# Kernel optimization log

Hardware: AMD Instinct MI355X
Metric: run time of the kernel (lower is better)

Reference implementation:

```python
import jax, jax.numpy as jnp
import numpy as np
import math

B, L = 2, 512
D_MODEL = 64
N_HEAD = 8
N_GLOBAL = 64
N_ITER = 2
DISTS = 4
K_RANK = 4
REG_H = 1.0
REG_Z = 1.0
NEG = -1e9


def setup_inputs() -> dict:
    key = jax.random.key(0)
    k1, k2, k3, k4 = jax.random.split(key, 4)
    x = jax.random.normal(k1, (B, L, D_MODEL), dtype=jnp.float32)
    mask = jnp.ones((B, L), dtype=jnp.int32)
    # nn.init.normal_ defaults (std=1)
    distribution_params = jax.random.normal(k2, (2 * DISTS, K_RANK), dtype=jnp.float32)
    ternary = jax.random.normal(k3, (K_RANK, D_MODEL, D_MODEL, N_HEAD), dtype=jnp.float32)
    # global_: std = 1/sqrt(d_model), single-channel -> heads dim = 1
    global_param = jax.random.normal(k4, (N_GLOBAL, D_MODEL, 1), dtype=jnp.float32) * (1.0 / math.sqrt(D_MODEL))
    return {"x": x, "mask": mask, "distribution_params": distribution_params,
            "ternary": ternary, "global_param": global_param}


def _softmax(s):
    return jax.nn.softmax(s, axis=-1)


def _distmask(distribution_params, n, dtype):
    # distance(i,j) = clip(i - j, -dists, dists); row 0 of params is zeros (distance 0)
    dist = jnp.arange(n)[:, None] - jnp.arange(n)[None, :]
    dist = jnp.clip(dist, -DISTS, DISTS)
    params = jnp.concatenate([jnp.zeros((1, K_RANK), dtype), distribution_params], axis=0)  # [2*dists+1, k]
    # torch negative indexing wraps; emulate explicitly
    idx = jnp.where(dist < 0, dist + 2 * DISTS + 1, dist)
    return params[idx].transpose(2, 0, 1)  # [k, n, n]


def reference(x, mask, distribution_params, ternary, global_param):
    bsz, n, d = x.shape
    mask1d = mask != 0                                   # [B, L]
    mask2d = mask1d[:, :, None] & mask1d[:, None, :]     # [B, L, L]
    inv2d = ~mask2d[:, None, :, :]                       # [B, 1, L, L] broadcast over heads
    inv1d = ~mask1d[:, None, :, None]                    # [B, 1, L, 1]

    distmask = _distmask(distribution_params, n, x.dtype)  # [k, L, L]

    unary = x
    q_z = unary
    for _ in range(N_ITER):
        # --- normalize Z beliefs (softmax over d_model states) ---
        Q_z = _softmax(q_z / REG_Z)                      # [B, L, d]
        # precompute decomposed tensor messages: M1[z,k,j,a,c] = sum_b Qz[z,j,b] T[k,a,b,c]
        M1 = jnp.einsum('zjb,kabc->zkjac', Q_z, ternary)  # [B, k, L, d, h]
        # --- H update (each head of token i picks a parent j) ---
        # s_h[z,c,i,j] = sum_{a,k} Qz[z,i,a] M1[z,k,j,a,c] distmask[k,i,j]
        s_h = jnp.einsum('zia,zkjac,kij->zcij', Q_z, M1, distmask)  # [B, h, L, L]
        s_h = jnp.where(inv2d, NEG, s_h)
        Q_h = _softmax(s_h / REG_H)                      # softmax over parents j
        # --- global H update (single channel): token i picks one of n_global global nodes ---
        s_g = jnp.einsum('zia,gac->zcig', Q_z, global_param)        # [B, 1, L, G]
        s_g = jnp.where(inv1d, NEG, s_g)
        Q_g = _softmax(s_g / REG_H)
        # --- Z update: messages from ternary factors in both roles + global factor ---
        g1 = jnp.einsum('zcij,zkjac,kij->zia', Q_h, M1, distmask)   # token as Z_i
        M2 = jnp.einsum('zjb,kbac->zkjac', Q_z, ternary)            # swapped roles
        g2 = jnp.einsum('zcji,zkjac,kji->zia', Q_h, M2, distmask)   # token as Z_j
        gg = jnp.einsum('zcig,gac->zia', Q_g, global_param)         # global message
        q_z = unary + g1 + g2 + gg
        # damping=0, stepsize=1 -> plain full update
    # output_prob=False -> unnormalized scores
    return q_z
```

## Files before the change

### kernel.cpp

```cpp
#include <hip/hip_runtime.h>

#define BB 2
#define LL 512
#define DD 64
#define HH 8
#define GG 64
#define KK 4
#define NEGV -1e9f
#define NSLOT 36

typedef unsigned short ushort_t;
typedef __attribute__((ext_vector_type(8))) short bf16x8;
typedef __attribute__((ext_vector_type(4))) float f32x4;
#define MFMA(a, b, c) __builtin_amdgcn_mfma_f32_16x16x32_bf16(a, b, c, 0, 0, 0)

__device__ __forceinline__ ushort_t f2b(float f) {
    unsigned int u = __float_as_uint(f);
    return (ushort_t)((u + 0x7FFFu + ((u >> 16) & 1u)) >> 16);
}
__device__ __forceinline__ float b2f(ushort_t s) {
    return __uint_as_float(((unsigned int)s) << 16);
}

__device__ __forceinline__ void stage64(ushort_t* dst, const ushort_t* src,
                                        int rowstride, int tid) {
#pragma unroll
    for (int g = tid; g < 512; g += 256) {
        int row = g >> 3, colg = g & 7;
        uint4 v = *reinterpret_cast<const uint4*>(&src[row * rowstride + (colg << 3)]);
        *reinterpret_cast<uint4*>(&dst[(row << 6) + ((colg ^ (row & 7)) << 3)]) = v;
    }
}
__device__ __forceinline__ bf16x8 frag(const ushort_t* s, int row, int col) {
    return *reinterpret_cast<const bf16x8*>(&s[(row << 6) + ((((col >> 3) ^ (row & 7))) << 3)]);
}
__device__ __forceinline__ bf16x8 maskfrag(bf16x8 v, int cnt, bool keep_prefix) {
    bf16x8 r;
#pragma unroll
    for (int u = 0; u < 8; ++u) {
        bool keep = keep_prefix ? (u < cnt) : (u >= cnt);
        r[u] = keep ? v[u] : (short)0;
    }
    return r;
}
__device__ __forceinline__ int iclamp(int v, int lo, int hi) {
    return v < lo ? lo : (v > hi ? hi : v);
}

__global__ __launch_bounds__(256) void k_prepT(const float* __restrict__ T,
                                               ushort_t* __restrict__ TB1,
                                               ushort_t* __restrict__ TB2) {
    int k = blockIdx.x >> 3, c = blockIdx.x & 7;
    int tid = threadIdx.x;
    for (int g = tid; g < 512; g += 256) {
        int a = g >> 3, b0 = (g & 7) * 8;
        ushort_t o1[8], o2[8];
#pragma unroll
        for (int u = 0; u < 8; ++u) {
            o1[u] = f2b(T[(((k * 64 + a) * 64) + b0 + u) * 8 + c]);
            o2[u] = f2b(T[(((k * 64 + b0 + u) * 64) + a) * 8 + c]);
        }
        size_t base = ((size_t)(k * 8 + c) * 64 + a) * 64 + b0;
        *reinterpret_cast<uint4*>(&TB1[base]) = *reinterpret_cast<uint4*>(o1);
        *reinterpret_cast<uint4*>(&TB2[base]) = *reinterpret_cast<uint4*>(o2);
    }
}

__global__ __launch_bounds__(256) void k_softmax_qz(const float* __restrict__ src,
                                                    float* __restrict__ Qz,
                                                    ushort_t* __restrict__ QzB) {
    int row = blockIdx.x * 4 + (threadIdx.x >> 6);
    int lane = threadIdx.x & 63;
    float v = src[row * DD + lane];
    float m = v;
#pragma unroll
    for (int o = 32; o > 0; o >>= 1) m = fmaxf(m, __shfl_xor(m, o, 64));
    float e = __expf(v - m);
    float s = e;
#pragma unroll
    for (int o = 32; o > 0; o >>= 1) s += __shfl_xor(s, o, 64);
    float r = e / s;
    Qz[row * DD + lane] = r;
    QzB[row * DD + lane] = f2b(r);
}

__global__ __launch_bounds__(256) void k_compute_M(const ushort_t* __restrict__ QzB,
        const ushort_t* __restrict__ TB1, const ushort_t* __restrict__ TB2,
        ushort_t* __restrict__ M1Nb, ushort_t* __restrict__ M2Nb) {
    int jt = blockIdx.x, c = blockIdx.y;
    int z = blockIdx.z >> 2, k = blockIdx.z & 3;
    __shared__ ushort_t sQ[4096], sB1[4096], sB2[4096];
    int tid = threadIdx.x;
    stage64(sQ, QzB + (size_t)(z * LL + jt * 64) * DD, DD, tid);
    size_t tb = (size_t)(k * 8 + c) * 4096;
    stage64(sB1, TB1 + tb, 64, tid);
    stage64(sB2, TB2 + tb, 64, tid);
    __syncthreads();
    int w = tid >> 6, lm = tid & 15, lg = (tid & 63) >> 4;
    f32x4 a1[4], a2[4];
#pragma unroll
    for (int nf = 0; nf < 4; ++nf) { a1[nf] = {0.f,0.f,0.f,0.f}; a2[nf] = {0.f,0.f,0.f,0.f}; }
#pragma unroll
    for (int ks = 0; ks < 2; ++ks) {
        int kc = ks * 32 + lg * 8;
        bf16x8 af = frag(sQ, w * 16 + lm, kc);
#pragma unroll
        for (int nf = 0; nf < 4; ++nf) {
            a1[nf] = MFMA(af, frag(sB1, nf * 16 + lm, kc), a1[nf]);
            a2[nf] = MFMA(af, frag(sB2, nf * 16 + lm, kc), a2[nf]);
        }
    }
    size_t base = (((size_t)z * KK + k) * HH + c) * LL;
#pragma unroll
    for (int nf = 0; nf < 4; ++nf)
#pragma unroll
        for (int r = 0; r < 4; ++r) {
            int j = jt * 64 + w * 16 + lg * 4 + r;
            int a = nf * 16 + lm;
            M1Nb[(base + j) * DD + a] = f2b(a1[nf][r]);
            M2Nb[(base + j) * DD + a] = f2b(a2[nf][r]);
        }
}

__global__ __launch_bounds__(256, 4) void k_collaux(const float* __restrict__ Qz,
        const ushort_t* __restrict__ M1Nb, const ushort_t* __restrict__ M2Nb,
        const float* __restrict__ dp, const float* __restrict__ gp, const int* __restrict__ mask,
        ushort_t* __restrict__ MPNb, ushort_t* __restrict__ MMNb,
        ushort_t* __restrict__ MP2Nb, ushort_t* __restrict__ MM2Nb,
        ushort_t* __restrict__ MPT, ushort_t* __restrict__ MMT,
        ushort_t* __restrict__ MP2T, ushort_t* __restrict__ MM2T,
        float* __restrict__ BAND, float* __restrict__ QG) {
    __shared__ __align__(16) ushort_t sT[4 * 64 * 65];
    int tid = threadIdx.x;
    int b = blockIdx.x;
    if (b < 128) {
        int jt = b & 7, zc = b >> 3;
        int z = zc >> 3, c = zc & 7;
        ushort_t* sP1 = sT;
        ushort_t* sM1 = sT + 64 * 65;
        ushort_t* sP2 = sT + 2 * 64 * 65;
        ushort_t* sM2 = sT + 3 * 64 * 65;
        float w4[4], w5[4];
#pragma unroll
        for (int k = 0; k < 4; ++k) { w4[k] = dp[12 + k]; w5[k] = dp[16 + k]; }
        size_t b0 = (((size_t)z * KK * HH + c) * LL + jt * 64) * DD;
        const size_t kstr = (size_t)HH * LL * DD;
        for (int g = tid; g < 512; g += 256) {
            int j = g >> 3, a0 = (g & 7) * 8;
            size_t o = b0 + (size_t)j * DD + a0;
            float p1[8] = {}, q1[8] = {}, p2[8] = {}, q2[8] = {};
#pragma unroll
            for (int k = 0; k < 4; ++k) {
                uint4 v1 = *reinterpret_cast<const uint4*>(&M1Nb[o + k * kstr]);
                uint4 v2 = *reinterpret_cast<const uint4*>(&M2Nb[o + k * kstr]);
                const ushort_t* s1 = reinterpret_cast<const ushort_t*>(&v1);
                const ushort_t* s2 = reinterpret_cast<const ushort_t*>(&v2);
#pragma unroll
                for (int u = 0; u < 8; ++u) {
                    float f1 = b2f(s1[u]), f2v = b2f(s2[u]);
                    p1[u] += w4[k] * f1; q1[u] += w5[k] * f1;
                    p2[u] += w4[k] * f2v; q2[u] += w5[k] * f2v;
                }
            }
            ushort_t t1[8], t2[8], t3[8], t4[8];
#pragma unroll
            for (int u = 0; u < 8; ++u) {
                t1[u] = f2b(p1[u]); t2[u] = f2b(q1[u]); t3[u] = f2b(p2[u]); t4[u] = f2b(q2[u]);
                sP1[(a0 + u) * 65 + j] = t1[u]; sM1[(a0 + u) * 65 + j] = t2[u];
                sP2[(a0 + u) * 65 + j] = t3[u]; sM2[(a0 + u) * 65 + j] = t4[u];
            }
            size_t on = ((size_t)zc * LL + jt * 64 + j) * DD + a0;
            *reinterpret_cast<uint4*>(&MPNb[on])  = *reinterpret_cast<uint4*>(t1);
            *reinterpret_cast<uint4*>(&MMNb[on])  = *reinterpret_cast<uint4*>(t2);
            *reinterpret_cast<uint4*>(&MP2Nb[on]) = *reinterpret_cast<uint4*>(t3);
            *reinterpret_cast<uint4*>(&MM2Nb[on]) = *reinterpret_cast<uint4*>(t4);
        }
        __syncthreads();
        for (int g = tid; g < 512; g += 256) {
            int a = g >> 3, j0 = (g & 7) * 8;
            ushort_t o1[8], o2[8], o3[8], o4[8];
#pragma unroll
            for (int u = 0; u < 8; ++u) {
                o1[u] = sP1[a * 65 + j0 + u]; o2[u] = sM1[a * 65 + j0 + u];
                o3[u] = sP2[a * 65 + j0 + u]; o4[u] = sM2[a * 65 + j0 + u];
            }
            size_t ot = ((size_t)zc * DD + a) * LL + jt * 64 + j0;
            *reinterpret_cast<uint4*>(&MPT[ot])  = *reinterpret_cast<uint4*>(o1);
            *reinterpret_cast<uint4*>(&MMT[ot])  = *reinterpret_cast<uint4*>(o2);
            *reinterpret_cast<uint4*>(&MP2T[ot]) = *reinterpret_cast<uint4*>(o3);
            *reinterpret_cast<uint4*>(&MM2T[ot]) = *reinterpret_cast<uint4*>(o4);
        }
    } else if (b < 2176) {
        int w = (b - 128) * 4 + (tid >> 6);
        int lane = tid & 63;
        int j = w & 511, c = (w >> 9) & 7, z = w >> 12;
        float m[4];
#pragma unroll
        for (int k = 0; k < 4; ++k)
            m[k] = b2f(M1Nb[((((size_t)z * KK + k) * HH + c) * LL + j) * DD + lane]);
        float out = 0.f;
#pragma unroll
        for (int d = -3; d <= 3; ++d) {
            int i = j + d;
            if (i < 0 || i >= LL) continue;
            int idx = d < 0 ? d + 9 : d;
            float t = 0.f;
            if (idx != 0) {
#pragma unroll
                for (int k = 0; k < 4; ++k) t += dp[(idx - 1) * 4 + k] * m[k];
            }
            float s = Qz[(z * LL + i) * DD + lane] * t;
#pragma unroll
            for (int o = 32; o > 0; o >>= 1) s += __shfl_xor(s, o, 64);
            if (lane == d + 3) out = s;
        }
        if (lane < 7) BAND[(size_t)w * 8 + lane] = out;
    } else {
        float* gpS = reinterpret_cast<float*>(sT);
#pragma unroll
        for (int idx = tid; idx < 4096; idx += 256) gpS[(idx >> 6) * 68 + (idx & 63)] = gp[idx];
        __syncthreads();
        int row = (b - 2176) * 4 + (tid >> 6);
        int g = tid & 63;
        float qv = Qz[row * DD + g];
        float s = 0.f;
#pragma unroll 8
        for (int a = 0; a < 64; ++a) s += __shfl(qv, a, 64) * gpS[g * 68 + a];
        if (mask[row] == 0) s = NEGV;
        float m = s;
#pragma unroll
        for (int o = 32; o > 0; o >>= 1) m = fmaxf(m, __shfl_xor(m, o, 64));
        float e = __expf(s - m);
        float sum = e;
#pragma unroll
        for (int o = 32; o > 0; o >>= 1) sum += __shfl_xor(sum, o, 64);
        QG[row * GG + g] = e / sum;
    }
}

__global__ __launch_bounds__(256, 2) void k_shsm32(const ushort_t* __restrict__ QzB,
        const ushort_t* __restrict__ MPNb, const ushort_t* __restrict__ MMNb,
        const float* __restrict__ BAND, const int* __restrict__ mask,
        ushort_t* __restrict__ SHB, ushort_t* __restrict__ SHBT) {
    int ih = blockIdx.x, zc = blockIdx.y;
    int it = ih >> 1, rh = ih & 1;
    int z = zc >> 3;
    int R0 = it * 64 + rh * 32;
    __shared__ ushort_t sA[2048];
    __shared__ ushort_t sB0[4096], sB1[4096], sBd[4096];
    __shared__ ushort_t tl[2][32 * 72];
    __shared__ float redA[2][32], redB[2][32];
    int tid = threadIdx.x;
    int w = tid >> 6, lm = tid & 15, lg = (tid & 63) >> 4;
    int rw = w & 1, cw = w >> 1;
    {
        int row = tid >> 3, colg = tid & 7;
        uint4 v = *reinterpret_cast<const uint4*>(
            &QzB[(size_t)(z * LL + R0 + row) * DD + (colg << 3)]);
        *reinterpret_cast<uint4*>(&sA[(row << 6) + ((colg ^ (row & 7)) << 3)]) = v;
    }
    f32x4 acc[4][4];
#pragma unroll
    for (int jl = 0; jl < 4; ++jl)
#pragma unroll
        for (int nf = 0; nf < 4; ++nf) acc[jl][nf] = {0.f, 0.f, 0.f, 0.f};
    int dstep = it & 3;
#pragma unroll
    for (int s = 0; s < 4; ++s) {
        __syncthreads();
        int jt0 = s, jt1 = 4 + s;
        const ushort_t* src0 = (it >= jt0) ? MPNb : MMNb;
        const ushort_t* src1 = (it >= jt1) ? MPNb : MMNb;
        stage64(sB0, src0 + ((size_t)zc * LL + jt0 * 64) * DD, DD, tid);
        stage64(sB1, src1 + ((size_t)zc * LL + jt1 * 64) * DD, DD, tid);
        if (s == dstep)
            stage64(sBd, MMNb + ((size_t)zc * LL + it * 64) * DD, DD, tid);
        __syncthreads();
        int jtg = cw ? jt1 : jt0;
        const ushort_t* sBx = cw ? sB1 : sB0;
#pragma unroll
        for (int ks = 0; ks < 2; ++ks) {
            int kc = ks * 32 + lg * 8;
            bf16x8 af = frag(sA, rw * 16 + lm, kc);
#pragma unroll
            for (int nf = 0; nf < 4; ++nf)
                acc[s][nf] = MFMA(af, frag(sBx, nf * 16 + lm, kc), acc[s][nf]);
        }
        if (jtg == it) {
            f32x4 accM[4];
#pragma unroll
            for (int nf = 0; nf < 4; ++nf) accM[nf] = {0.f, 0.f, 0.f, 0.f};
#pragma unroll
            for (int ks = 0; ks < 2; ++ks) {
                int kc = ks * 32 + lg * 8;
                bf16x8 af = frag(sA, rw * 16 + lm, kc);
#pragma unroll
                for (int nf = 0; nf < 4; ++nf)
                    accM[nf] = MFMA(af, frag(sBd, nf * 16 + lm, kc), accM[nf]);
            }
#pragma unroll
            for (int nf = 0; nf < 4; ++nf)
#pragma unroll
                for (int r = 0; r < 4; ++r) {
                    int i = R0 + rw * 16 + lg * 4 + r;
                    int j = it * 64 + nf * 16 + lm;
                    if (i <= j) acc[s][nf][r] = accM[nf][r];
                }
        }
    }
    int mi[4];
#pragma unroll
    for (int r = 0; r < 4; ++r) mi[r] = mask[z * LL + R0 + rw * 16 + lg * 4 + r];
#pragma unroll
    for (int jl = 0; jl < 4; ++jl) {
        int jtg = cw * 4 + jl;
#pragma unroll
        for (int nf = 0; nf < 4; ++nf) {
            int j = jtg * 64 + nf * 16 + lm;
            int mjv = mask[z * LL + j];
#pragma unroll
            for (int r = 0; r < 4; ++r) {
                int i = R0 + rw * 16 + lg * 4 + r;
                int d = i - j;
                float v = acc[jl][nf][r];
                if (d >= -3 && d <= 3) v = BAND[((size_t)zc * LL + j) * 8 + (d + 3)];
                if (!(mi[r] && mjv)) v = NEGV;
                acc[jl][nf][r] = v;
            }
        }
    }
    float gm[4], gs[4], inv[4];
#pragma unroll
    for (int r = 0; r < 4; ++r) {
        float m = -1e30f;
#pragma unroll
        for (int jl = 0; jl < 4; ++jl)
#pragma unroll
            for (int nf = 0; nf < 4; ++nf) m = fmaxf(m, acc[jl][nf][r]);
#pragma unroll
        for (int o = 1; o < 16; o <<= 1) m = fmaxf(m, __shfl_xor(m, o, 64));
        gm[r] = m;
    }
    if (lm == 0) {
#pragma unroll
        for (int r = 0; r < 4; ++r) redA[cw][rw * 16 + lg * 4 + r] = gm[r];
    }
    __syncthreads();
#pragma unroll
    for (int r = 0; r < 4; ++r)
        gm[r] = fmaxf(gm[r], redA[cw ^ 1][rw * 16 + lg * 4 + r]);
#pragma unroll
    for (int r = 0; r < 4; ++r) {
        float s = 0.f;
#pragma unroll
        for (int jl = 0; jl < 4; ++jl)
#pragma unroll
            for (int nf = 0; nf < 4; ++nf) {
                float e = __expf(acc[jl][nf][r] - gm[r]);
                acc[jl][nf][r] = e;
                s += e;
            }
#pragma unroll
        for (int o = 1; o < 16; o <<= 1) s += __shfl_xor(s, o, 64);
        gs[r] = s;
    }
    if (lm == 0) {
#pragma unroll
        for (int r = 0; r < 4; ++r) redB[cw][rw * 16 + lg * 4 + r] = gs[r];
    }
    __syncthreads();
#pragma unroll
    for (int r = 0; r < 4; ++r)
        inv[r] = 1.f / (gs[r] + redB[cw ^ 1][rw * 16 + lg * 4 + r]);
#pragma unroll
    for (int jl = 0; jl < 4; ++jl) {
        __syncthreads();
#pragma unroll
        for (int nf = 0; nf < 4; ++nf)
#pragma unroll
            for (int r = 0; r < 4; ++r)
                tl[cw][(rw * 16 + lg * 4 + r) * 72 + nf * 16 + lm] =
                    f2b(acc[jl][nf][r] * inv[r]);
        __syncthreads();
#pragma unroll
        for (int g = tid; g < 512; g += 256) {
            int cwg = g >> 8, rem = g & 255;
            int jtg = cwg * 4 + jl;
            int i_loc = rem >> 3, gj = rem & 7;
            ushort_t tmp[8];
#pragma unroll
            for (int u = 0; u < 8; ++u) tmp[u] = tl[cwg][i_loc * 72 + gj * 8 + u];
            *reinterpret_cast<uint4*>(
                &SHB[((size_t)zc * LL + R0 + i_loc) * LL + jtg * 64 + gj * 8]) =
                *reinterpret_cast<uint4*>(tmp);
        }
#pragma unroll
        for (int g = tid; g < 512; g += 256) {
            int cwg = g >> 8, rem = g & 255;
            int jtg = cwg * 4 + jl;
            int j_loc = rem >> 2, gi = rem & 3;
            ushort_t tmp2[8];
#pragma unroll
            for (int u = 0; u < 8; ++u) tmp2[u] = tl[cwg][(gi * 8 + u) * 72 + j_loc];
            *reinterpret_cast<uint4*>(
                &SHBT[((size_t)zc * LL + jtg * 64 + j_loc) * LL + R0 + gi * 8]) =
                *reinterpret_cast<uint4*>(tmp2);
        }
    }
}

__global__ __launch_bounds__(256, 4) void k_g12corr(const ushort_t* __restrict__ SHB,
        const ushort_t* __restrict__ SHBT,
        const ushort_t* __restrict__ MPT, const ushort_t* __restrict__ MMT,
        const ushort_t* __restrict__ MP2T, const ushort_t* __restrict__ MM2T,
        const ushort_t* __restrict__ M1Nb, const ushort_t* __restrict__ M2Nb,
        const ushort_t* __restrict__ MPNb, const ushort_t* __restrict__ MMNb,
        const ushort_t* __restrict__ MP2Nb, const ushort_t* __restrict__ MM2Nb,
        const float* __restrict__ dp, float* __restrict__ PG) {
    __shared__ ushort_t sSH[4096], sM[4096];
    int tid = threadIdx.x;
    int b = blockIdx.x;
    if (b < 512) {
        int it = b & 7, jc = (b >> 3) & 1, zcw = b >> 4;
        int which = zcw >> 4;
        int z = (zcw >> 3) & 1, c = zcw & 7;
        const ushort_t* Amat = which ? SHBT : SHB;
        const ushort_t* TP = which ? MP2T : MPT;
        const ushort_t* TM = which ? MM2T : MMT;
        int w = tid >> 6, lm = tid & 15, lg = (tid & 63) >> 4;
        f32x4 acc[4];
#pragma unroll
        for (int nf = 0; nf < 4; ++nf) acc[nf] = {0.f,0.f,0.f,0.f};
        size_t shbase = ((size_t)(z * HH + c) * LL + it * 64) * LL;
        size_t mbase  = ((size_t)(z * HH + c) * DD) * LL;
        for (int js = 0; js < 4; ++js) {
            int j0 = jc * 256 + js * 64;
            bool dg = (j0 == it * 64);
            bool useP = which == 0 ? (j0 < it * 64) : (j0 > it * 64);
            __syncthreads();
            stage64(sSH, Amat + shbase + j0, LL, tid);
            stage64(sM, (dg ? TP : (useP ? TP : TM)) + mbase + j0, LL, tid);
            __syncthreads();
            for (int pass = 0; pass < (dg ? 2 : 1); ++pass) {
                if (pass == 1) {
                    __syncthreads();
                    stage64(sM, TM + mbase + j0, LL, tid);
                    __syncthreads();
                }
#pragma unroll
                for (int ks = 0; ks < 2; ++ks) {
                    int kc = ks * 32 + lg * 8;
                    int jb = j0 + kc;
                    bf16x8 af = frag(sSH, w * 16 + lm, kc);
                    if (dg) {
                        int i = it * 64 + w * 16 + lm;
                        int cnt = (which == 0) ? iclamp(i - jb, 0, 8) : iclamp(i + 1 - jb, 0, 8);
                        af = maskfrag(af, cnt, (pass == 0) == (which == 0));
                    }
#pragma unroll
                    for (int nf = 0; nf < 4; ++nf)
                        acc[nf] = MFMA(af, frag(sM, nf * 16 + lm, kc), acc[nf]);
                }
            }
        }
        int slot = which * 16 + c * 2 + jc;
#pragma unroll
        for (int nf = 0; nf < 4; ++nf)
#pragma unroll
            for (int r = 0; r < 4; ++r) {
                int i = it * 64 + w * 16 + lg * 4 + r;
                int a = nf * 16 + lm;
                PG[((size_t)(slot * BB + z) * LL + i) * DD + a] = acc[nf][r];
            }
    } else {
        int bid = b - 512;
        int which = bid >> 9; bid &= 511;
        int w = bid * 4 + (tid >> 6);
        int lane = tid & 63;
        int ch = w & 1, i = (w >> 1) & 511, z = w >> 10;
        const ushort_t* Mx = which ? M2Nb : M1Nb;
        const ushort_t* MPb = which ? MP2Nb : MPNb;
        const ushort_t* MMb = which ? MM2Nb : MMNb;
        float acc = 0.f;
        for (int cc = 0; cc < 4; ++cc) {
            int c = ch * 4 + cc;
#pragma unroll
            for (int d = -3; d <= 3; ++d) {
                int j = which ? i + d : i - d;
                if (j < 0 || j >= LL) continue;
                float qh = which ? b2f(SHB[(((size_t)z * HH + c) * LL + j) * LL + i])
                                 : b2f(SHB[(((size_t)z * HH + c) * LL + i) * LL + j]);
                int idx = d < 0 ? d + 9 : d;
                float e = 0.f;
                if (idx != 0) {
#pragma unroll
                    for (int k = 0; k < 4; ++k)
                        e += dp[(idx - 1) * 4 + k] *
                             b2f(Mx[((((size_t)z * KK + k) * HH + c) * LL + j) * DD + lane]);
                }
                const ushort_t* mb = (d > 0) ? MPb : MMb;
                float mn = b2f(mb[(((size_t)z * HH + c) * LL + j) * DD + lane]);
                acc += qh * (e - mn);
            }
        }
        int slot = 32 + which * 2 + ch;
        PG[(((size_t)slot * BB + z) * LL + i) * DD + lane] = acc;
    }
}

__global__ __launch_bounds__(256) void k_update(const float* __restrict__ x, const float* __restrict__ PG,
                         const float* __restrict__ QG, const float* __restrict__ gp,
                         float* __restrict__ outq) {
    __shared__ __align__(16) float gpS[64][68];
    int tid = threadIdx.x;
#pragma unroll
    for (int idx = tid; idx < 4096; idx += 256) gpS[idx >> 6][idx & 63] = gp[idx];
    __syncthreads();
    int row = blockIdx.x * 4 + (tid >> 6);
    int a = tid & 63;
    float acc = x[row * DD + a];
    float qgv = QG[row * GG + a];
#pragma unroll 8
    for (int g = 0; g < 64; ++g) acc += __shfl(qgv, g, 64) * gpS[g][a];
#pragma unroll 6
    for (int s = 0; s < NSLOT; ++s) acc += PG[((size_t)s * BB * LL + row) * DD + a];
    outq[row * DD + a] = acc;
}

extern "C" void kernel_launch(void* const* d_in, const int* in_sizes, int n_in,
                              void* d_out, int out_size, void* d_ws, size_t ws_size,
                              hipStream_t stream) {
    const float* x    = (const float*)d_in[0];
    const int*   mask = (const int*)d_in[1];
    const float* dp   = (const float*)d_in[2];
    const float* T    = (const float*)d_in[3];
    const float* gp   = (const float*)d_in[4];
    float* out = (float*)d_out;

    float* p = (float*)d_ws;
    float* Qz = p;                        p += 65536;
    ushort_t* QzB = (ushort_t*)p;         p += 32768;
    ushort_t* TB1 = (ushort_t*)p;         p += 65536;
    ushort_t* TB2 = (ushort_t*)p;         p += 65536;
    ushort_t* M1Nb = (ushort_t*)p;        p += 1048576;
    ushort_t* M2Nb = (ushort_t*)p;        p += 1048576;
    ushort_t* MPNb  = (ushort_t*)p;       p += 262144;
    ushort_t* MMNb  = (ushort_t*)p;       p += 262144;
    ushort_t* MP2Nb = (ushort_t*)p;       p += 262144;
    ushort_t* MM2Nb = (ushort_t*)p;       p += 262144;
    ushort_t* MPT   = (ushort_t*)p;       p += 262144;
    ushort_t* MMT   = (ushort_t*)p;       p += 262144;
    ushort_t* MP2T  = (ushort_t*)p;       p += 262144;
    ushort_t* MM2T  = (ushort_t*)p;       p += 262144;
    float* BAND = p;                      p += 65536;
    ushort_t* SHB  = (ushort_t*)p;        p += 2097152;
    ushort_t* SHBT = (ushort_t*)p;        p += 2097152;
    float* QG   = p;                      p += 65536;
    float* PG   = p;                      p += (size_t)NSLOT * 65536;
    float* QZ1  = p;                      p += 65536;

    hipLaunchKernelGGL(k_prepT, dim3(32), dim3(256), 0, stream, T, TB1, TB2);

    const float* qsrc = x;
    for (int iter = 0; iter < 2; ++iter) {
        float* qdst = (iter == 0) ? QZ1 : out;
        hipLaunchKernelGGL(k_softmax_qz, dim3(256), dim3(256), 0, stream, qsrc, Qz, QzB);
        hipLaunchKernelGGL(k_compute_M, dim3(8, 8, 8), dim3(256), 0, stream, QzB, TB1, TB2, M1Nb, M2Nb);
        hipLaunchKernelGGL(k_collaux, dim3(2432), dim3(256), 0, stream, Qz, M1Nb, M2Nb, dp, gp, mask,
                           MPNb, MMNb, MP2Nb, MM2Nb, MPT, MMT, MP2T, MM2T, BAND, QG);
        hipLaunchKernelGGL(k_shsm32, dim3(16, 16), dim3(256), 0, stream, QzB, MPNb, MMNb, BAND, mask,
                           SHB, SHBT);
        hipLaunchKernelGGL(k_g12corr, dim3(1536), dim3(256), 0, stream, SHB, SHBT,
                           MPT, MMT, MP2T, MM2T, M1Nb, M2Nb,
                           MPNb, MMNb, MP2Nb, MM2Nb, dp, PG);
        hipLaunchKernelGGL(k_update, dim3(256), dim3(256), 0, stream, x, PG, QG, gp, qdst);
        qsrc = qdst;
    }
}
```

Before: 138.5 us.

## Stage tiles via global_load_lds and fuse Qz softmax into update kernel

Replaces the register-staged global-to-LDS copies in several kernels with direct global_load_lds 16-byte loads. The XOR swizzle moves to the source addresses so the LDS destination stays linear per wave. The first-iteration update kernel now also computes the next Qz softmax, removing one launch and the intermediate QZ1 round trip. The direct-to-LDS path depends on correct LDS address and alignment semantics, and waits on it may interact with barriers differently.

```diff
diff --git a/kernel.cpp b/kernel.cpp
--- a/kernel.cpp
+++ b/kernel.cpp
@@ -14,6 +14,9 @@
 typedef __attribute__((ext_vector_type(4))) float f32x4;
 #define MFMA(a, b, c) __builtin_amdgcn_mfma_f32_16x16x32_bf16(a, b, c, 0, 0, 0)
 
+typedef const __attribute__((address_space(1))) unsigned int* gptr_t;
+typedef __attribute__((address_space(3))) unsigned int* lptr_t;
+
 __device__ __forceinline__ ushort_t f2b(float f) {
     unsigned int u = __float_as_uint(f);
     return (ushort_t)((u + 0x7FFFu + ((u >> 16) & 1u)) >> 16);
@@ -22,13 +25,22 @@
     return __uint_as_float(((unsigned int)s) << 16);
 }
 
-__device__ __forceinline__ void stage64(ushort_t* dst, const ushort_t* src,
-                                        int rowstride, int tid) {
-#pragma unroll
-    for (int g = tid; g < 512; g += 256) {
+__device__ __forceinline__ void gll16(const ushort_t* g, const ushort_t* l) {
+    __builtin_amdgcn_global_load_lds(
+        (gptr_t)(unsigned long long)g,
+        (lptr_t)(unsigned int)(unsigned long long)l,
+        16, 0, 0);
+}
+
+__device__ __forceinline__ void stage64a(ushort_t* dst, const ushort_t* src,
+                                         int rowstride, int tid) {
+    int lane = tid & 63, w = tid >> 6;
+#pragma unroll
+    for (int h = 0; h < 2; ++h) {
+        int g = h * 256 + w * 64 + lane;
         int row = g >> 3, colg = g & 7;
-        uint4 v = *reinterpret_cast<const uint4*>(&src[row * rowstride + (colg << 3)]);
-        *reinterpret_cast<uint4*>(&dst[(row << 6) + ((colg ^ (row & 7)) << 3)]) = v;
+        gll16(src + (size_t)row * rowstride + ((colg ^ (row & 7)) << 3),
+              dst + (size_t)(h * 256 + w * 64) * 8);
     }
 }
 __device__ __forceinline__ bf16x8 frag(const ushort_t* s, int row, int col) {
@@ -89,12 +101,12 @@
         ushort_t* __restrict__ M1Nb, ushort_t* __restrict__ M2Nb) {
     int jt = blockIdx.x, c = blockIdx.y;
     int z = blockIdx.z >> 2, k = blockIdx.z & 3;
-    __shared__ ushort_t sQ[4096], sB1[4096], sB2[4096];
+    __shared__ __align__(16) ushort_t sQ[4096], sB1[4096], sB2[4096];
     int tid = threadIdx.x;
-    stage64(sQ, QzB + (size_t)(z * LL + jt * 64) * DD, DD, tid);
+    stage64a(sQ, QzB + (size_t)(z * LL + jt * 64) * DD, DD, tid);
     size_t tb = (size_t)(k * 8 + c) * 4096;
-    stage64(sB1, TB1 + tb, 64, tid);
-    stage64(sB2, TB2 + tb, 64, tid);
+    stage64a(sB1, TB1 + tb, 64, tid);
+    stage64a(sB2, TB2 + tb, 64, tid);
     __syncthreads();
     int w = tid >> 6, lm = tid & 15, lg = (tid & 63) >> 4;
     f32x4 a1[4], a2[4];
@@ -246,18 +258,17 @@
     int it = ih >> 1, rh = ih & 1;
     int z = zc >> 3;
     int R0 = it * 64 + rh * 32;
-    __shared__ ushort_t sA[2048];
-    __shared__ ushort_t sB0[4096], sB1[4096], sBd[4096];
-    __shared__ ushort_t tl[2][32 * 72];
+    __shared__ __align__(16) ushort_t sA[2048];
+    __shared__ __align__(16) ushort_t sB0[4096], sB1[4096], sBd[4096];
+    __shared__ __align__(16) ushort_t tl[2][32 * 72];
     __shared__ float redA[2][32], redB[2][32];
     int tid = threadIdx.x;
     int w = tid >> 6, lm = tid & 15, lg = (tid & 63) >> 4;
     int rw = w & 1, cw = w >> 1;
     {
         int row = tid >> 3, colg = tid & 7;
-        uint4 v = *reinterpret_cast<const uint4*>(
-            &QzB[(size_t)(z * LL + R0 + row) * DD + (colg << 3)]);
-        *reinterpret_cast<uint4*>(&sA[(row << 6) + ((colg ^ (row & 7)) << 3)]) = v;
+        gll16(&QzB[(size_t)(z * LL + R0 + row) * DD + ((colg ^ (row & 7)) << 3)],
+              sA + (size_t)(w * 64) * 8);
     }
     f32x4 acc[4][4];
 #pragma unroll
@@ -271,10 +282,10 @@
         int jt0 = s, jt1 = 4 + s;
         const ushort_t* src0 = (it >= jt0) ? MPNb : MMNb;
         const ushort_t* src1 = (it >= jt1) ? MPNb : MMNb;
-        stage64(sB0, src0 + ((size_t)zc * LL + jt0 * 64) * DD, DD, tid);
-        stage64(sB1, src1 + ((size_t)zc * LL + jt1 * 64) * DD, DD, tid);
+        stage64a(sB0, src0 + ((size_t)zc * LL + jt0 * 64) * DD, DD, tid);
+        stage64a(sB1, src1 + ((size_t)zc * LL + jt1 * 64) * DD, DD, tid);
         if (s == dstep)
-            stage64(sBd, MMNb + ((size_t)zc * LL + it * 64) * DD, DD, tid);
+            stage64a(sBd, MMNb + ((size_t)zc * LL + it * 64) * DD, DD, tid);
         __syncthreads();
         int jtg = cw ? jt1 : jt0;
         const ushort_t* sBx = cw ? sB1 : sB0;
@@ -417,7 +428,7 @@
         const ushort_t* __restrict__ MPNb, const ushort_t* __restrict__ MMNb,
         const ushort_t* __restrict__ MP2Nb, const ushort_t* __restrict__ MM2Nb,
         const float* __restrict__ dp, float* __restrict__ PG) {
-    __shared__ ushort_t sSH[4096], sM[4096];
+    __shared__ __align__(16) ushort_t sSH[4096], sM[4096];
     int tid = threadIdx.x;
     int b = blockIdx.x;
     if (b < 512) {
@@ -438,13 +449,13 @@
             bool dg = (j0 == it * 64);
             bool useP = which == 0 ? (j0 < it * 64) : (j0 > it * 64);
             __syncthreads();
-            stage64(sSH, Amat + shbase + j0, LL, tid);
-            stage64(sM, (dg ? TP : (useP ? TP : TM)) + mbase + j0, LL, tid);
+            stage64a(sSH, Amat + shbase + j0, LL, tid);
+            stage64a(sM, (dg ? TP : (useP ? TP : TM)) + mbase + j0, LL, tid);
             __syncthreads();
             for (int pass = 0; pass < (dg ? 2 : 1); ++pass) {
                 if (pass == 1) {
                     __syncthreads();
-                    stage64(sM, TM + mbase + j0, LL, tid);
+                    stage64a(sM, TM + mbase + j0, LL, tid);
                     __syncthreads();
                 }
 #pragma unroll
@@ -508,9 +519,38 @@
     }
 }
 
-__global__ __launch_bounds__(256) void k_update(const float* __restrict__ x, const float* __restrict__ PG,
-                         const float* __restrict__ QG, const float* __restrict__ gp,
-                         float* __restrict__ outq) {
+__global__ __launch_bounds__(256) void k_update_sm(const float* __restrict__ x,
+                         const float* __restrict__ PG, const float* __restrict__ QG,
+                         const float* __restrict__ gp,
+                         float* __restrict__ Qz, ushort_t* __restrict__ QzB) {
+    __shared__ __align__(16) float gpS[64][68];
+    int tid = threadIdx.x;
+#pragma unroll
+    for (int idx = tid; idx < 4096; idx += 256) gpS[idx >> 6][idx & 63] = gp[idx];
+    __syncthreads();
+    int row = blockIdx.x * 4 + (tid >> 6);
+    int a = tid & 63;
+    float acc = x[row * DD + a];
+    float qgv = QG[row * GG + a];
+#pragma unroll 8
+    for (int g = 0; g < 64; ++g) acc += __shfl(qgv, g, 64) * gpS[g][a];
+#pragma unroll 6
+    for (int s = 0; s < NSLOT; ++s) acc += PG[((size_t)s * BB * LL + row) * DD + a];
+    float m = acc;
+#pragma unroll
+    for (int o = 32; o > 0; o >>= 1) m = fmaxf(m, __shfl_xor(m, o, 64));
+    float e = __expf(acc - m);
+    float s2 = e;
+#pragma unroll
+    for (int o = 32; o > 0; o >>= 1) s2 += __shfl_xor(s2, o, 64);
+    float r = e / s2;
+    Qz[row * DD + a] = r;
+    QzB[row * DD + a] = f2b(r);
+}
+
+__global__ __launch_bounds__(256) void k_update_fin(const float* __restrict__ x,
+                         const float* __restrict__ PG, const float* __restrict__ QG,
+                         const float* __restrict__ gp, float* __restrict__ outq) {
     __shared__ __align__(16) float gpS[64][68];
     int tid = threadIdx.x;
 #pragma unroll
@@ -557,14 +597,11 @@
     ushort_t* SHBT = (ushort_t*)p;        p += 2097152;
     float* QG   = p;                      p += 65536;
     float* PG   = p;                      p += (size_t)NSLOT * 65536;
-    float* QZ1  = p;                      p += 65536;
 
     hipLaunchKernelGGL(k_prepT, dim3(32), dim3(256), 0, stream, T, TB1, TB2);
-
-    const float* qsrc = x;
+    hipLaunchKernelGGL(k_softmax_qz, dim3(256), dim3(256), 0, stream, x, Qz, QzB);
+
     for (int iter = 0; iter < 2; ++iter) {
-        float* qdst = (iter == 0) ? QZ1 : out;
-        hipLaunchKernelGGL(k_softmax_qz, dim3(256), dim3(256), 0, stream, qsrc, Qz, QzB);
         hipLaunchKernelGGL(k_compute_M, dim3(8, 8, 8), dim3(256), 0, stream, QzB, TB1, TB2, M1Nb, M2Nb);
         hipLaunchKernelGGL(k_collaux, dim3(2432), dim3(256), 0, stream, Qz, M1Nb, M2Nb, dp, gp, mask,
                            MPNb, MMNb, MP2Nb, MM2Nb, MPT, MMT, MP2T, MM2T, BAND, QG);
@@ -573,7 +610,9 @@
         hipLaunchKernelGGL(k_g12corr, dim3(1536), dim3(256), 0, stream, SHB, SHBT,
                            MPT, MMT, MP2T, MM2T, M1Nb, M2Nb,
                            MPNb, MMNb, MP2Nb, MM2Nb, dp, PG);
-        hipLaunchKernelGGL(k_update, dim3(256), dim3(256), 0, stream, x, PG, QG, gp, qdst);
-        qsrc = qdst;
-    }
-}
+        if (iter == 0)
+            hipLaunchKernelGGL(k_update_sm, dim3(256), dim3(256), 0, stream, x, PG, QG, gp, Qz, QzB);
+        else
+            hipLaunchKernelGGL(k_update_fin, dim3(256), dim3(256), 0, stream, x, PG, QG, gp, out);
+    }
+}
```

Measured after the change: 134.4 us. 3.0% less time.
